# Kernel optimization log

Measured on AMD Instinct MI355X. Metric: run time of the kernel, lower is better.

Reference implementation:

```python
import jax, jax.numpy as jnp
import numpy as np

B, S, H = 4, 4096, 2880
E, K = 32, 4


def setup_inputs() -> dict:
    key = jax.random.key(0)
    k1, k2 = jax.random.split(key)
    hidden_states = jax.random.normal(k1, (B, S, H), dtype=jnp.float32)
    # router weight, scaled like a typical init (std ~ 1/sqrt(H))
    weight = jax.random.normal(k2, (E, H), dtype=jnp.float32) / np.sqrt(H)
    bias = jnp.zeros((E,), dtype=jnp.float32)
    return {"hidden_states": hidden_states, "weight": weight, "bias": bias}


def reference(hidden_states, weight, bias):
    b, s, h = hidden_states.shape
    x = hidden_states.reshape(-1, h)                     # [T, H]
    logits = jnp.einsum('th,eh->te', x, weight) + bias   # [T, E]
    # select top-k logits (sorted descending), then softmax over the subset
    topk_logits, topk_idx = jax.lax.top_k(logits, K)     # [T, K]
    topk_weight = jax.nn.softmax(topk_logits.astype(jnp.float32), axis=-1)
    return topk_idx, topk_weight
```

## Files before the change

kernel.cpp:

```cpp
#include <hip/hip_runtime.h>
#include <math.h>

#define H_DIM 2880
#define E_NUM 32
#define TOPK 4
#define NCH 16
#define HCHUNK 180
#define TB 512
#define KS 12
#define NS 15

typedef float vf16 __attribute__((ext_vector_type(16)));

#define GLD16(gp, lp)                                                  \
    __builtin_amdgcn_global_load_lds(                                  \
        (const __attribute__((address_space(1))) void*)(gp),           \
        (__attribute__((address_space(3))) void*)(lp), 16, 0, 0)

__global__ void transpose_w(const float* __restrict__ w, float* __restrict__ wt) {
    __shared__ float tile[32][33];
    const int h0 = blockIdx.x * 32;
    const int tx = threadIdx.x;
    const int ty = threadIdx.y;
    tile[tx][ty] = w[ty * H_DIM + h0 + tx];
    __syncthreads();
    wt[(h0 + ty) * E_NUM + tx] = tile[ty][tx];
}

__global__ __launch_bounds__(256, 2) void partial_logits(
    const float* __restrict__ x, const float* __restrict__ wt,
    float* __restrict__ part, int T) {
    __shared__ float xs[2][TB * KS];
    const int tid = threadIdx.x;
    const int t0 = blockIdx.x * TB;
    const int k0 = blockIdx.y * HCHUNK;
    const int wave = tid >> 6, lane = tid & 63;

    const float* g[6];
    int lo[6];
#pragma unroll
    for (int i = 0; i < 6; ++i) {
        int f = wave * 384 + i * 64 + lane;
        int r = f / 3, c = f % 3;
        g[i] = x + (size_t)(t0 + r) * H_DIM + k0 + c * 4;
        lo[i] = f * 4;
    }

    float acc[64];
#pragma unroll
    for (int e = 0; e < 64; ++e) acc[e] = 0.f;

    const vf16* wtv = (const vf16*)wt;

#pragma unroll
    for (int i = 0; i < 6; ++i) GLD16(g[i], &xs[0][lo[i]]);

    for (int s = 0; s < NS; ++s) {
        __syncthreads();
        if (s + 1 < NS) {
#pragma unroll
            for (int i = 0; i < 6; ++i)
                GLD16(g[i] + (size_t)(s + 1) * KS, &xs[(s + 1) & 1][lo[i]]);
        }
        const float* xa = &xs[s & 1][tid * KS];
        const float* xb = &xs[s & 1][(tid + 256) * KS];
        const int kb = k0 + s * KS;
#pragma unroll
        for (int kk = 0; kk < 3; ++kk) {
            float4 va = *(const float4*)&xa[kk * 4];
            float4 vb = *(const float4*)&xb[kk * 4];
#pragma unroll
            for (int c = 0; c < 4; ++c) {
                float fa = (&va.x)[c], fb = (&vb.x)[c];
                int kg = kb + kk * 4 + c;
                vf16 w0 = wtv[kg * 2 + 0];
                vf16 w1 = wtv[kg * 2 + 1];
#pragma unroll
                for (int e = 0; e < 16; ++e) {
                    acc[e]      += fa * w0[e];
                    acc[16 + e] += fa * w1[e];
                    acc[32 + e] += fb * w0[e];
                    acc[48 + e] += fb * w1[e];
                }
            }
        }
    }

    float4* oa = (float4*)(part + ((size_t)blockIdx.y * T + t0 + tid) * E_NUM);
    float4* ob = (float4*)(part + ((size_t)blockIdx.y * T + t0 + tid + 256) * E_NUM);
#pragma unroll
    for (int j = 0; j < 8; ++j) {
        oa[j] = make_float4(acc[j * 4], acc[j * 4 + 1], acc[j * 4 + 2], acc[j * 4 + 3]);
        ob[j] = make_float4(acc[32 + j * 4], acc[32 + j * 4 + 1],
                            acc[32 + j * 4 + 2], acc[32 + j * 4 + 3]);
    }
}

__global__ __launch_bounds__(256) void topk_softmax(
    const float* __restrict__ part, const float* __restrict__ bias,
    float* __restrict__ out, int T) {
    __shared__ float red[3][64][36];
    const int tid = threadIdx.x, g = tid >> 6, l = tid & 63;
    const int t = blockIdx.x * 64 + l;

    float s[E_NUM];
#pragma unroll
    for (int e = 0; e < E_NUM; ++e) s[e] = 0.f;
#pragma unroll
    for (int q = 0; q < 4; ++q) {
        const int hc = g * 4 + q;
        const float4* p4 = (const float4*)(part + ((size_t)hc * T + t) * E_NUM);
#pragma unroll
        for (int j = 0; j < 8; ++j) {
            float4 p = p4[j];
            s[j * 4] += p.x; s[j * 4 + 1] += p.y;
            s[j * 4 + 2] += p.z; s[j * 4 + 3] += p.w;
        }
    }
    if (g > 0) {
#pragma unroll
        for (int j = 0; j < 8; ++j)
            *(float4*)&red[g - 1][l][j * 4] =
                make_float4(s[j * 4], s[j * 4 + 1], s[j * 4 + 2], s[j * 4 + 3]);
    }
    __syncthreads();
    if (g == 0) {
        float logit[E_NUM];
        const float4* b4 = (const float4*)bias;
#pragma unroll
        for (int j = 0; j < 8; ++j) {
            float4 b = b4[j];
            logit[j * 4] = b.x; logit[j * 4 + 1] = b.y;
            logit[j * 4 + 2] = b.z; logit[j * 4 + 3] = b.w;
        }
#pragma unroll
        for (int e = 0; e < E_NUM; ++e)
            logit[e] += s[e] + red[0][l][e] + red[1][l][e] + red[2][l][e];

        int idx[TOPK];
        float val[TOPK];
#pragma unroll
        for (int k = 0; k < TOPK; ++k) {
            float best = -INFINITY;
            int bi = 0;
#pragma unroll
            for (int e = 0; e < E_NUM; ++e) {
                bool taken = false;
                for (int p = 0; p < k; ++p) taken = taken || (idx[p] == e);
                float v = logit[e];
                if (!taken && v > best) { best = v; bi = e; }
            }
            idx[k] = bi;
            val[k] = best;
        }
        float ex[TOPK], sum = 0.f;
#pragma unroll
        for (int k = 0; k < TOPK; ++k) { ex[k] = expf(val[k] - val[0]); sum += ex[k]; }
        float inv = 1.f / sum;
#pragma unroll
        for (int k = 0; k < TOPK; ++k) {
            out[(size_t)t * 4 + k] = (float)idx[k];
            out[(size_t)T * 4 + (size_t)t * 4 + k] = ex[k] * inv;
        }
    }
}

extern "C" void kernel_launch(void* const* d_in, const int* in_sizes, int n_in,
                              void* d_out, int out_size, void* d_ws, size_t ws_size,
                              hipStream_t stream) {
    const float* x    = (const float*)d_in[0];
    const float* w    = (const float*)d_in[1];
    const float* bias = (const float*)d_in[2];
    float* out = (float*)d_out;

    const int T = in_sizes[0] / H_DIM;

    float* part = (float*)d_ws;
    float* wt = part + (size_t)NCH * T * E_NUM;

    transpose_w<<<dim3(H_DIM / 32), dim3(32, 32), 0, stream>>>(w, wt);
    partial_logits<<<dim3(T / TB, NCH), 256, 0, stream>>>(x, wt, part, T);
    topk_softmax<<<dim3(T / 64), 256, 0, stream>>>(part, bias, out, T);
}
```

Baseline: 307.2 us.

## Shrink per-thread logit tile and split experts across thread halves for occupancy

Rewrites the partial-logits kernel so each thread computes one token against 16 experts instead of two tokens against all 32. Tokens per block drop from 512 to 128, the hidden dimension is split into 12 chunks of 240, and launch bounds allow 4 blocks per SM. Only three waves issue the LDS DMA loads, and each stage now loads and syncs in one step instead of prefetching the next stage. The goal is more blocks and waves in flight and less register pressure. The cost is less reuse of each loaded x value and load latency that is no longer explicitly overlapped with compute.

```diff
diff --git a/kernel.cpp b/kernel.cpp
--- a/kernel.cpp
+++ b/kernel.cpp
@@ -4,11 +4,11 @@
 #define H_DIM 2880
 #define E_NUM 32
 #define TOPK 4
-#define NCH 16
-#define HCHUNK 180
-#define TB 512
+#define NCH 12
+#define HCHUNK 240
+#define TT 128
 #define KS 12
-#define NS 15
+#define NS 20
 
 typedef float vf16 __attribute__((ext_vector_type(16)));
 
@@ -27,73 +27,61 @@
     wt[(h0 + ty) * E_NUM + tx] = tile[ty][tx];
 }
 
-__global__ __launch_bounds__(256, 2) void partial_logits(
+__global__ __launch_bounds__(256, 4) void partial_logits(
     const float* __restrict__ x, const float* __restrict__ wt,
     float* __restrict__ part, int T) {
-    __shared__ float xs[2][TB * KS];
+    __shared__ float xs[2][TT * KS];
     const int tid = threadIdx.x;
-    const int t0 = blockIdx.x * TB;
+    const int t0 = blockIdx.x * TT;
     const int k0 = blockIdx.y * HCHUNK;
     const int wave = tid >> 6, lane = tid & 63;
+    const int half = tid >> 7;
+    const int tok = tid & 127;
 
-    const float* g[6];
-    int lo[6];
+    const bool dma = (wave < 3);
+    const float* g[2];
+    int lo[2];
+    if (dma) {
 #pragma unroll
-    for (int i = 0; i < 6; ++i) {
-        int f = wave * 384 + i * 64 + lane;
-        int r = f / 3, c = f % 3;
-        g[i] = x + (size_t)(t0 + r) * H_DIM + k0 + c * 4;
-        lo[i] = f * 4;
+        for (int i = 0; i < 2; ++i) {
+            int f = wave * 128 + i * 64 + lane;
+            int r = f / 3, c = f % 3;
+            g[i] = x + (size_t)(t0 + r) * H_DIM + k0 + c * 4;
+            lo[i] = f * 4;
+        }
     }
 
-    float acc[64];
+    float acc[16];
 #pragma unroll
-    for (int e = 0; e < 64; ++e) acc[e] = 0.f;
-
-    const vf16* wtv = (const vf16*)wt;
-
-#pragma unroll
-    for (int i = 0; i < 6; ++i) GLD16(g[i], &xs[0][lo[i]]);
+    for (int e = 0; e < 16; ++e) acc[e] = 0.f;
 
     for (int s = 0; s < NS; ++s) {
+        if (dma) {
+#pragma unroll
+            for (int i = 0; i < 2; ++i)
+                GLD16(g[i] + (size_t)s * KS, &xs[s & 1][lo[i]]);
+        }
         __syncthreads();
-        if (s + 1 < NS) {
-#pragma unroll
-            for (int i = 0; i < 6; ++i)
-                GLD16(g[i] + (size_t)(s + 1) * KS, &xs[(s + 1) & 1][lo[i]]);
-        }
-        const float* xa = &xs[s & 1][tid * KS];
-        const float* xb = &xs[s & 1][(tid + 256) * KS];
+        const float* xrow = &xs[s & 1][tok * KS];
         const int kb = k0 + s * KS;
 #pragma unroll
         for (int kk = 0; kk < 3; ++kk) {
-            float4 va = *(const float4*)&xa[kk * 4];
-            float4 vb = *(const float4*)&xb[kk * 4];
+            float4 xv = *(const float4*)&xrow[kk * 4];
 #pragma unroll
             for (int c = 0; c < 4; ++c) {
-                float fa = (&va.x)[c], fb = (&vb.x)[c];
+                float xk = (&xv.x)[c];
                 int kg = kb + kk * 4 + c;
-                vf16 w0 = wtv[kg * 2 + 0];
-                vf16 w1 = wtv[kg * 2 + 1];
+                vf16 wv = *(const vf16*)(wt + (size_t)kg * E_NUM + half * 16);
 #pragma unroll
-                for (int e = 0; e < 16; ++e) {
-                    acc[e]      += fa * w0[e];
-                    acc[16 + e] += fa * w1[e];
-                    acc[32 + e] += fb * w0[e];
-                    acc[48 + e] += fb * w1[e];
-                }
+                for (int e = 0; e < 16; ++e) acc[e] += xk * wv[e];
             }
         }
     }
 
-    float4* oa = (float4*)(part + ((size_t)blockIdx.y * T + t0 + tid) * E_NUM);
-    float4* ob = (float4*)(part + ((size_t)blockIdx.y * T + t0 + tid + 256) * E_NUM);
+    float4* o = (float4*)(part + ((size_t)blockIdx.y * T + t0 + tok) * E_NUM + half * 16);
 #pragma unroll
-    for (int j = 0; j < 8; ++j) {
-        oa[j] = make_float4(acc[j * 4], acc[j * 4 + 1], acc[j * 4 + 2], acc[j * 4 + 3]);
-        ob[j] = make_float4(acc[32 + j * 4], acc[32 + j * 4 + 1],
-                            acc[32 + j * 4 + 2], acc[32 + j * 4 + 3]);
-    }
+    for (int j = 0; j < 4; ++j)
+        o[j] = make_float4(acc[j * 4], acc[j * 4 + 1], acc[j * 4 + 2], acc[j * 4 + 3]);
 }
 
 __global__ __launch_bounds__(256) void topk_softmax(
@@ -107,8 +95,8 @@
 #pragma unroll
     for (int e = 0; e < E_NUM; ++e) s[e] = 0.f;
 #pragma unroll
-    for (int q = 0; q < 4; ++q) {
-        const int hc = g * 4 + q;
+    for (int q = 0; q < 3; ++q) {
+        const int hc = g * 3 + q;
         const float4* p4 = (const float4*)(part + ((size_t)hc * T + t) * E_NUM);
 #pragma unroll
         for (int j = 0; j < 8; ++j) {
@@ -179,6 +167,6 @@
     float* wt = part + (size_t)NCH * T * E_NUM;
 
     transpose_w<<<dim3(H_DIM / 32), dim3(32, 32), 0, stream>>>(w, wt);
-    partial_logits<<<dim3(T / TB, NCH), 256, 0, stream>>>(x, wt, part, T);
+    partial_logits<<<dim3(T / TT, NCH), 256, 0, stream>>>(x, wt, part, T);
     topk_softmax<<<dim3(T / 64), 256, 0, stream>>>(part, bias, out, T);
 }
```

Measured after the change: 425.1 us. 38.4% more time.
